# Kernel tuning notes

Hardware: AMD Instinct MI355X
Metric: run time of the kernel (lower is better)

Reference implementation:

```python
import jax, jax.numpy as jnp
import numpy as np

N_HEADS = 16
NEG_INF = -1e9


def setup_inputs() -> dict:
    key = jax.random.key(0)
    ks = jax.random.split(key, 8)
    B, S, D = 2, 2048, 1024
    HD = D // N_HEADS
    x = jax.random.normal(ks[0], (B, S, D), dtype=jnp.float32)
    # RoPE frequencies (llama-style): theta = 10000^(-2i/head_dim)
    inv_freq = 1.0 / (10000.0 ** (np.arange(0, HD, 2, dtype=np.float32) / HD))  # [HD//2]
    angles = np.arange(S, dtype=np.float32)[:, None] * inv_freq[None, :]        # [S, HD//2]
    freqs_cos = jnp.asarray(np.cos(angles))
    freqs_sin = jnp.asarray(np.sin(angles))
    # additive causal mask [1,1,S,S]
    mask = jnp.where(np.tril(np.ones((S, S), dtype=bool)), 0.0, NEG_INF).astype(jnp.float32)[None, None]
    scale = 0.02
    wq = jax.random.normal(ks[1], (D, D), dtype=jnp.float32) * scale
    wk = jax.random.normal(ks[2], (D, D), dtype=jnp.float32) * scale
    wv = jax.random.normal(ks[3], (D, D), dtype=jnp.float32) * scale
    wo = jax.random.normal(ks[4], (D, D), dtype=jnp.float32) * scale
    return {"x": x, "freqs_cos": freqs_cos, "freqs_sin": freqs_sin, "mask": mask,
            "wq": wq, "wk": wk, "wv": wv, "wo": wo}


def _rope(t, cos, sin):
    # t: [B,S,H,HD]; cos/sin: [S,HD//2]; complex mult (t0 + i t1) * (cos + i sin)
    b, s, h, hd = t.shape
    tr = t.reshape(b, s, h, hd // 2, 2)
    t0, t1 = tr[..., 0], tr[..., 1]
    c = cos[None, :, None, :]
    sn = sin[None, :, None, :]
    out = jnp.stack([t0 * c - t1 * sn, t0 * sn + t1 * c], axis=-1)
    return out.reshape(b, s, h, hd)


def reference(x, freqs_cos, freqs_sin, mask, wq, wk, wv, wo):
    b, s, d = x.shape
    hd = d // N_HEADS
    # torch Linear: y = x @ W.T
    xq = (x @ wq.T).reshape(b, s, N_HEADS, hd)
    xk = (x @ wk.T).reshape(b, s, N_HEADS, hd)
    xv = (x @ wv.T).reshape(b, s, N_HEADS, hd)
    xq = _rope(xq, freqs_cos, freqs_sin)
    xk = _rope(xk, freqs_cos, freqs_sin)
    # [B,H,S,S] scores
    scores = jnp.einsum('bqhd,bkhd->bhqk', xq, xk) / jnp.sqrt(jnp.asarray(hd, x.dtype))
    scores = scores + mask
    probs = jax.nn.softmax(scores.astype(jnp.float32), axis=-1).astype(x.dtype)
    out = jnp.einsum('bhqk,bkhd->bqhd', probs, xv).reshape(b, s, d)
    return out @ wo.T
```

## Files before the change

kernel.cpp:

```cpp
#include <hip/hip_runtime.h>
#include <hip/hip_bf16.h>
#include <cstdint>

typedef __attribute__((ext_vector_type(4))) float f32x4;
typedef __attribute__((ext_vector_type(8))) short s16x8;
typedef __attribute__((ext_vector_type(4))) unsigned short u16x4;
typedef unsigned short u16;
typedef unsigned int u32;
typedef unsigned long long u64;

__device__ __forceinline__ float b2f(u16 u){ u32 v = ((u32)u)<<16; return __builtin_bit_cast(float, v); }
__device__ __forceinline__ u16 f2b(float f){
  __hip_bfloat16 h = __float2bfloat16(f);
  return __builtin_bit_cast(u16, h);
}

__device__ __forceinline__ void gld16(const void* g, void* l){
  __builtin_amdgcn_global_load_lds((const __attribute__((address_space(1))) void*)g,
                                   (__attribute__((address_space(3))) void*)l, 16, 0, 0);
}

__device__ __forceinline__ f32x4 mfma16(s16x8 a, s16x8 b, f32x4 c){
  return __builtin_amdgcn_mfma_f32_16x16x32_bf16(a, b, c, 0, 0, 0);
}

#define WS_XB   0u
#define WS_WQ   (4u<<20)
#define WS_WK   (5u<<20)
#define WS_WV   (6u<<20)
#define WS_WO   (7u<<20)
#define WS_Q    (8u<<20)
#define WS_K    (12u<<20)
#define WS_VT   (16u<<20)
#define WS_AO   (20u<<20)

#define QSCALE 0.18033688f

__global__ __launch_bounds__(256) void k_convert(const float* __restrict__ x,
    const float* __restrict__ wq, const float* __restrict__ wk,
    const float* __restrict__ wv, const float* __restrict__ wo,
    u16* __restrict__ ws){
  u32 idx = blockIdx.x*256u + threadIdx.x;
  const float* src; u16* dst;
  if (idx < (1u<<20)) { src = x + (u64)idx*4u; dst = ws + WS_XB + (u64)idx*4u; }
  else {
    u32 widx = idx - (1u<<20);
    u32 wsel = widx >> 18;
    u32 off  = (widx & ((1u<<18)-1u)) * 4u;
    const float* sp = (wsel==0u)?wq:(wsel==1u)?wk:(wsel==2u)?wv:wo;
    src = sp + off; dst = ws + WS_WQ + (u64)wsel*(1u<<20) + off;
  }
  f32x4 v = *(const f32x4*)src;
  u16x4 o = { f2b(v[0]), f2b(v[1]), f2b(v[2]), f2b(v[3]) };
  *(u16x4*)dst = o;
}

__global__ __launch_bounds__(256,2) void k_gemm(u16* __restrict__ ws, float* __restrict__ out,
    const float* __restrict__ fc, const float* __restrict__ fs, int pass){
  __shared__ char sm[65536];
  const u32 tid = threadIdx.x;
  const u32 w = tid>>6, l = tid&63u, g = l>>4, li = l&15u;
  const u32 wr = w>>1, wc = w&1u;
  u32 bx = blockIdx.x;

  const u16 *Ap, *Bp; u32 arow0, brow0; int mode;
  if (pass == 0) {
    u32 seg = bx >> 8, b2 = bx & 255u;
    if (seg < 2u) {
      Ap = ws + WS_XB; Bp = ws + (seg ? WS_WK : WS_WQ);
      arow0 = (b2 >> 3) * 128u; brow0 = (b2 & 7u) * 128u; mode = (int)seg;
    } else {
      Ap = ws + WS_WV; Bp = ws + WS_XB;
      arow0 = (b2 >> 5) * 128u; brow0 = (b2 & 31u) * 128u; mode = 2;
    }
  } else {
    Ap = ws + WS_AO; Bp = ws + WS_WO;
    arow0 = (bx >> 3) * 128u; brow0 = (bx & 7u) * 128u; mode = 3;
  }

  f32x4 acc[4][4];
  #pragma unroll
  for (u32 m=0;m<4;++m)
    #pragma unroll
    for (u32 n=0;n<4;++n) acc[m][n] = 0.0f;

  auto STAGE_G = [&](u32 s, u32 t){
    const u32 k0 = t*64u;
    #pragma unroll
    for (u32 j = 0; j < 4u; ++j) {
      u32 p = w*4096u + j*1024u + l*16u;
      u32 row = p >> 7, colb = p & 127u;
      u32 cS = colb ^ ((row & 7u) << 4);
      gld16(Ap + (u64)(arow0 + row)*1024u + k0 + (cS>>1), sm + s*32768u + w*4096u + j*1024u);
      gld16(Bp + (u64)(brow0 + row)*1024u + k0 + (cS>>1), sm + s*32768u + 16384u + w*4096u + j*1024u);
    }
  };

  STAGE_G(0u, 0u);
  __syncthreads();

  u32 cur = 0u;
  for (u32 t = 0; t < 16u; ++t) {
    if (t + 1u < 16u) STAGE_G(cur^1u, t+1u);
    const u32 cb = cur*32768u;
    s16x8 af[2][4], bf[2][4];
    #pragma unroll
    for (u32 kk=0;kk<2u;++kk){
      #pragma unroll
      for (u32 m=0;m<4;++m){
        u32 row = wr*64u + m*16u + li;
        af[kk][m] = *(const s16x8*)(sm + cb + row*128u + ((kk*64u + g*16u) ^ ((row&7u)<<4)));
      }
      #pragma unroll
      for (u32 n=0;n<4;++n){
        u32 row = wc*64u + n*16u + li;
        bf[kk][n] = *(const s16x8*)(sm + cb + 16384u + row*128u + ((kk*64u + g*16u) ^ ((row&7u)<<4)));
      }
    }
    #pragma unroll
    for (u32 kk=0;kk<2u;++kk)
      #pragma unroll
      for (u32 m=0;m<4;++m)
        #pragma unroll
        for (u32 n=0;n<4;++n)
          acc[m][n] = mfma16(af[kk][m], bf[kk][n], acc[m][n]);
    __syncthreads();
    cur ^= 1u;
  }

  u16* qdst = ws + WS_Q; u16* kdst = ws + WS_K; u16* vtd = ws + WS_VT;
  if (mode <= 1) {
    #pragma unroll
    for (u32 m=0;m<4;++m)
      #pragma unroll
      for (u32 n=0;n<4;++n)
        #pragma unroll
        for (u32 q=0;q<4;++q){
          u32 row = wr*64u + m*16u + 4u*g + q;
          u32 colb = (wc*64u + n*16u + li)*2u;
          *(u16*)(sm + row*256u + (colb ^ ((row&7u)<<4))) = f2b(acc[m][n][q]);
        }
    __syncthreads();
    u32 row = tid >> 1, half = tid & 1u;
    u32 r = arow0 + row;
    u32 b = r >> 11, s = r & 2047u;
    u32 h = (brow0 >> 6) + half;
    float qs = (mode==0) ? QSCALE : 1.0f;
    u16* d = ((mode==0) ? qdst : kdst) + (u64)(((b<<4)+h)*2048u + s)*64u;
    #pragma unroll
    for (u32 u0=0; u0<8u; ++u0){
      s16x8 cv = *(const s16x8*)(sm + row*256u + ((half*128u + u0*16u) ^ ((row&7u)<<4)));
      f32x4 cvv = *(const f32x4*)(fc + s*32u + u0*4u);
      f32x4 svv = *(const f32x4*)(fs + s*32u + u0*4u);
      s16x8 o;
      #pragma unroll
      for (u32 i=0;i<4;++i){
        float t0 = b2f((u16)cv[2*i]), t1 = b2f((u16)cv[2*i+1]);
        o[2*i]   = (short)f2b((t0*cvv[i] - t1*svv[i])*qs);
        o[2*i+1] = (short)f2b((t0*svv[i] + t1*cvv[i])*qs);
      }
      *(s16x8*)(d + u0*8u) = o;
    }
  } else {
    #pragma unroll
    for (u32 m=0;m<4;++m){
      u32 r0 = arow0 + wr*64u + m*16u + 4u*g;
      #pragma unroll
      for (u32 n=0;n<4;++n){
        u32 c = brow0 + wc*64u + n*16u + li;
        #pragma unroll
        for (u32 q=0;q<4;++q){
          float v = acc[m][n][q];
          u32 r = r0 + q;
          if (mode == 2) vtd[(u64)r*4096u + c] = f2b(v);
          else           out[(u64)r*1024u + c] = v;
        }
      }
    }
  }
}

__global__ __launch_bounds__(256) void k_attn(u16* __restrict__ ws){
  __shared__ char sm[40960];
  const u32 tid = threadIdx.x;
  const u32 w = tid>>6, l = tid&63u, g = l>>4, li = l&15u;
  u32 bx = blockIdx.x;
  u32 qt = 31u - (bx >> 5);
  u32 bh = bx & 31u;
  u32 b = bh >> 4, h = bh & 15u;
  const u16* Q  = ws + WS_Q + (u64)bh*2048u*64u;
  const u16* Kp = ws + WS_K + (u64)bh*2048u*64u;
  const u16* Vt = ws + WS_VT + (u64)(h*64u)*4096u + b*2048u;
  u16* AO = ws + WS_AO;
  const u32 qw = qt*64u + w*16u;

  s16x8 qa[2];
  #pragma unroll
  for (u32 kk=0;kk<2;++kk)
    qa[kk] = *(const s16x8*)(Q + (u64)(qw + li)*64u + kk*32u + g*8u);

  s16x8 ones;
  #pragma unroll
  for (u32 i=0;i<8;++i) ones[i] = (short)0x3F80;

  f32x4 o[4]; f32x4 lsum;
  #pragma unroll
  for (u32 n=0;n<4;++n) o[n] = 0.0f;
  lsum = 0.0f;

  char* pl = sm + 32768 + w*2048u;
  const u32 nt = qt + 1u;

  auto STAGE = [&](u32 s, u32 kvb){
    #pragma unroll
    for (u32 j=0;j<2u;++j){
      u32 p = (w*2u+j)*1024u + l*16u;
      u32 row = p >> 7, colb = p & 127u;
      u32 cS = colb ^ ((row & 7u) << 4);
      gld16(Kp + (u64)(kvb + row)*64u + (cS>>1), sm + s*16384u + (w*2u+j)*1024u);
      gld16(Vt + (u64)row*4096u + kvb + (cS>>1), sm + s*16384u + 8192u + (w*2u+j)*1024u);
    }
  };

  STAGE(0u, 0u);
  __syncthreads();

  u32 cur = 0u;
  for (u32 t = 0; t < nt; ++t) {
    const u32 kvb = t*64u;
    if (t + 1u < nt) STAGE(cur^1u, kvb + 64u);
    const u32 cb = cur*16384u;

    f32x4 sv[4];
    #pragma unroll
    for (u32 n=0;n<4;++n) sv[n] = 0.0f;
    #pragma unroll
    for (u32 n=0;n<4;++n){
      u32 kvr = n*16u + li;
      #pragma unroll
      for (u32 kk=0;kk<2u;++kk){
        s16x8 kf = *(const s16x8*)(sm + cb + kvr*128u + ((kk*64u + g*16u) ^ ((kvr&7u)<<4)));
        sv[n] = mfma16(qa[kk], kf, sv[n]);
      }
    }
    if (t == nt - 1u) {
      #pragma unroll
      for (u32 n=0;n<4;++n)
        #pragma unroll
        for (u32 q=0;q<4;++q){
          u32 qr = qw + 4u*g + q;
          u32 kc = kvb + n*16u + li;
          if (kc > qr) sv[n][q] = -1e9f;
        }
    }
    #pragma unroll
    for (u32 n=0;n<4;++n)
      #pragma unroll
      for (u32 q=0;q<4;++q){
        u32 row = 4u*g + q;
        *(u16*)(pl + row*128u + (((n*16u + li)*2u) ^ ((row&7u)<<4))) = f2b(exp2f(sv[n][q]));
      }
    #pragma unroll
    for (u32 kk=0;kk<2u;++kk){
      s16x8 pa = *(const s16x8*)(pl + li*128u + ((kk*64u + g*16u) ^ ((li&7u)<<4)));
      lsum = mfma16(pa, ones, lsum);
      #pragma unroll
      for (u32 n=0;n<4;++n){
        u32 hr = n*16u + li;
        s16x8 vf = *(const s16x8*)(sm + cb + 8192u + hr*128u + ((kk*64u + g*16u) ^ ((hr&7u)<<4)));
        o[n] = mfma16(pa, vf, o[n]);
      }
    }
    __syncthreads();
    cur ^= 1u;
  }

  #pragma unroll
  for (u32 q=0;q<4;++q){
    float inv = 1.0f / lsum[q];
    u32 qr = qw + 4u*g + q;
    #pragma unroll
    for (u32 n=0;n<4;++n){
      u32 hd = n*16u + li;
      AO[((u64)(b*2048u + qr))*1024u + h*64u + hd] = f2b(o[n][q] * inv);
    }
  }
}

extern "C" void kernel_launch(void* const* d_in, const int* in_sizes, int n_in,
                              void* d_out, int out_size, void* d_ws, size_t ws_size,
                              hipStream_t stream) {
  const float* x  = (const float*)d_in[0];
  const float* fc = (const float*)d_in[1];
  const float* fs = (const float*)d_in[2];
  const float* wq = (const float*)d_in[4];
  const float* wk = (const float*)d_in[5];
  const float* wv = (const float*)d_in[6];
  const float* wo = (const float*)d_in[7];
  u16* ws = (u16*)d_ws;
  float* out = (float*)d_out;

  k_convert<<<8192, 256, 0, stream>>>(x, wq, wk, wv, wo, ws);
  k_gemm  <<<768,  256, 0, stream>>>(ws, out, fc, fs, 0);
  k_attn  <<<1024, 256, 0, stream>>>(ws);
  k_gemm  <<<256,  256, 0, stream>>>(ws, out, fc, fs, 1);
}
```

Baseline: 109.5 us.

## Split long causal attention rows across two blocks and merge partials

Query tiles 16-31 now have their KV range split into two halves, each processed by a separate block. This raises the attention grid from 1024 to 1536 blocks and evens out per-block work under the causal mask. Unnormalized partial outputs (bf16) and row sums go to workspace, and a new combine kernel sums them and normalizes. In exchange it adds a kernel launch, extra global traffic for the partials, and bf16 rounding of the partial outputs. It also reuses workspace regions (the start of ws and the WQ area) as scratch, assuming they are dead by this point.

```diff
diff --git a/kernel.cpp b/kernel.cpp
--- a/kernel.cpp
+++ b/kernel.cpp
@@ -185,8 +185,12 @@
   const u32 tid = threadIdx.x;
   const u32 w = tid>>6, l = tid&63u, g = l>>4, li = l&15u;
   u32 bx = blockIdx.x;
-  u32 qt = 31u - (bx >> 5);
+  u32 j = bx >> 5;
   u32 bh = bx & 31u;
+  u32 qt, t0, t1; bool split;
+  if (j < 16u)      { qt = 16u + j;  t0 = 0u;  t1 = 16u;      split = true;  }
+  else if (j < 32u) { qt = 47u - j;  t0 = 16u; t1 = qt + 1u;  split = true;  }
+  else              { qt = 47u - j;  t0 = 0u;  t1 = qt + 1u;  split = false; }
   u32 b = bh >> 4, h = bh & 15u;
   const u16* Q  = ws + WS_Q + (u64)bh*2048u*64u;
   const u16* Kp = ws + WS_K + (u64)bh*2048u*64u;
@@ -209,26 +213,25 @@
   lsum = 0.0f;
 
   char* pl = sm + 32768 + w*2048u;
-  const u32 nt = qt + 1u;
 
   auto STAGE = [&](u32 s, u32 kvb){
     #pragma unroll
-    for (u32 j=0;j<2u;++j){
-      u32 p = (w*2u+j)*1024u + l*16u;
+    for (u32 jj=0;jj<2u;++jj){
+      u32 p = (w*2u+jj)*1024u + l*16u;
       u32 row = p >> 7, colb = p & 127u;
       u32 cS = colb ^ ((row & 7u) << 4);
-      gld16(Kp + (u64)(kvb + row)*64u + (cS>>1), sm + s*16384u + (w*2u+j)*1024u);
-      gld16(Vt + (u64)row*4096u + kvb + (cS>>1), sm + s*16384u + 8192u + (w*2u+j)*1024u);
+      gld16(Kp + (u64)(kvb + row)*64u + (cS>>1), sm + s*16384u + (w*2u+jj)*1024u);
+      gld16(Vt + (u64)row*4096u + kvb + (cS>>1), sm + s*16384u + 8192u + (w*2u+jj)*1024u);
     }
   };
 
-  STAGE(0u, 0u);
+  STAGE(0u, t0*64u);
   __syncthreads();
 
   u32 cur = 0u;
-  for (u32 t = 0; t < nt; ++t) {
+  for (u32 t = t0; t < t1; ++t) {
     const u32 kvb = t*64u;
-    if (t + 1u < nt) STAGE(cur^1u, kvb + 64u);
+    if (t + 1u < t1) STAGE(cur^1u, kvb + 64u);
     const u32 cb = cur*16384u;
 
     f32x4 sv[4];
@@ -243,7 +246,7 @@
         sv[n] = mfma16(qa[kk], kf, sv[n]);
       }
     }
-    if (t == nt - 1u) {
+    if (t == qt) {
       #pragma unroll
       for (u32 n=0;n<4;++n)
         #pragma unroll
@@ -275,16 +278,51 @@
     cur ^= 1u;
   }
 
-  #pragma unroll
-  for (u32 q=0;q<4;++q){
-    float inv = 1.0f / lsum[q];
-    u32 qr = qw + 4u*g + q;
-    #pragma unroll
-    for (u32 n=0;n<4;++n){
-      u32 hd = n*16u + li;
-      AO[((u64)(b*2048u + qr))*1024u + h*64u + hd] = f2b(o[n][q] * inv);
-    }
-  }
+  if (split) {
+    u32 set = (bh*16u + (qt - 16u))*2u + (t0 ? 1u : 0u);
+    u16* po = ws + (u64)set*4096u;
+    float* plm = (float*)(ws + WS_WQ) + set*64u;
+    #pragma unroll
+    for (u32 q=0;q<4;++q){
+      u32 rl = w*16u + 4u*g + q;
+      #pragma unroll
+      for (u32 n=0;n<4;++n)
+        po[rl*64u + n*16u + li] = f2b(o[n][q]);
+      if (li == 0u) plm[rl] = lsum[q];
+    }
+  } else {
+    #pragma unroll
+    for (u32 q=0;q<4;++q){
+      float inv = 1.0f / lsum[q];
+      u32 qr = qw + 4u*g + q;
+      #pragma unroll
+      for (u32 n=0;n<4;++n){
+        u32 hd = n*16u + li;
+        AO[((u64)(b*2048u + qr))*1024u + h*64u + hd] = f2b(o[n][q] * inv);
+      }
+    }
+  }
+}
+
+__global__ __launch_bounds__(256) void k_combine(u16* __restrict__ ws){
+  u32 idx = blockIdx.x*256u + threadIdx.x;
+  u32 g8 = idx & 7u;
+  u32 r  = (idx >> 3) & 63u;
+  u32 s2 = idx >> 9;
+  const u16* poA = ws + (u64)(s2*2u)*4096u + r*64u + g8*8u;
+  const u16* poB = poA + 4096u;
+  const float* plm = (float*)(ws + WS_WQ);
+  float inv = 1.0f / (plm[(s2*2u)*64u + r] + plm[(s2*2u+1u)*64u + r]);
+  s16x8 a = *(const s16x8*)poA;
+  s16x8 c = *(const s16x8*)poB;
+  s16x8 o;
+  #pragma unroll
+  for (u32 i=0;i<8;++i)
+    o[i] = (short)f2b((b2f((u16)a[i]) + b2f((u16)c[i])) * inv);
+  u32 bh = s2 >> 4, qt = 16u + (s2 & 15u);
+  u32 b = bh >> 4, h = bh & 15u;
+  u32 qrow = qt*64u + r;
+  *(s16x8*)(ws + WS_AO + (u64)(b*2048u + qrow)*1024u + h*64u + g8*8u) = o;
 }
 
 extern "C" void kernel_launch(void* const* d_in, const int* in_sizes, int n_in,
@@ -301,7 +339,8 @@
   float* out = (float*)d_out;
 
   k_convert<<<8192, 256, 0, stream>>>(x, wq, wk, wv, wo, ws);
-  k_gemm  <<<768,  256, 0, stream>>>(ws, out, fc, fs, 0);
-  k_attn  <<<1024, 256, 0, stream>>>(ws);
-  k_gemm  <<<256,  256, 0, stream>>>(ws, out, fc, fs, 1);
-}
+  k_gemm   <<<768,  256, 0, stream>>>(ws, out, fc, fs, 0);
+  k_attn   <<<1536, 256, 0, stream>>>(ws);
+  k_combine<<<1024, 256, 0, stream>>>(ws);
+  k_gemm   <<<256,  256, 0, stream>>>(ws, out, fc, fs, 1);
+}
```

New measurement: 114.8 us. +4.8%, slower.

## Store K/V tiles in MFMA fragment order and transpose QK^T to pack P writes

Applied to the files above, without the earlier changes.

The K and V tiles are now staged into shared memory already laid out in MFMA fragment order, so each lane reads its fragment at a fixed lane*16 offset with no XOR swizzle arithmetic. The score MFMA swaps operands to compute S^T, letting each lane convert four probabilities with packed bf16 conversion and write them as one 8-byte store instead of sixteen 2-byte stores. Launch bounds add a minimum of 4 blocks per CU to limit register use. The risks are LDS bank conflicts in the new unswizzled layout, and register spills from holding all eight K fragments at once under the tighter occupancy bound.

```diff
diff --git a/kernel.cpp b/kernel.cpp
--- a/kernel.cpp
+++ b/kernel.cpp
@@ -5,6 +5,7 @@
 typedef __attribute__((ext_vector_type(4))) float f32x4;
 typedef __attribute__((ext_vector_type(8))) short s16x8;
 typedef __attribute__((ext_vector_type(4))) unsigned short u16x4;
+typedef __attribute__((ext_vector_type(2))) unsigned int u32x2;
 typedef unsigned short u16;
 typedef unsigned int u32;
 typedef unsigned long long u64;
@@ -180,7 +181,7 @@
   }
 }
 
-__global__ __launch_bounds__(256) void k_attn(u16* __restrict__ ws){
+__global__ __launch_bounds__(256,4) void k_attn(u16* __restrict__ ws){
   __shared__ char sm[40960];
   const u32 tid = threadIdx.x;
   const u32 w = tid>>6, l = tid&63u, g = l>>4, li = l&15u;
@@ -211,14 +212,20 @@
   char* pl = sm + 32768 + w*2048u;
   const u32 nt = qt + 1u;
 
+  const u32 f0 = w*2u;
+  u32 kof[2], vof[2];
+  #pragma unroll
+  for (u32 j=0;j<2u;++j){
+    u32 f = f0 + j;
+    kof[j] = ((f>>1)*16u + li)*64u  + (f&1u)*32u + g*8u;
+    vof[j] = ((f>>1)*16u + li)*4096u + (f&1u)*32u + g*8u;
+  }
   auto STAGE = [&](u32 s, u32 kvb){
     #pragma unroll
     for (u32 j=0;j<2u;++j){
-      u32 p = (w*2u+j)*1024u + l*16u;
-      u32 row = p >> 7, colb = p & 127u;
-      u32 cS = colb ^ ((row & 7u) << 4);
-      gld16(Kp + (u64)(kvb + row)*64u + (cS>>1), sm + s*16384u + (w*2u+j)*1024u);
-      gld16(Vt + (u64)row*4096u + kvb + (cS>>1), sm + s*16384u + 8192u + (w*2u+j)*1024u);
+      u32 f = f0 + j;
+      gld16(Kp + (u64)kvb*64u + kof[j], sm + s*16384u + f*1024u);
+      gld16(Vt + (u64)vof[j] + kvb,     sm + s*16384u + 8192u + f*1024u);
     }
   };
 
@@ -229,45 +236,47 @@
   for (u32 t = 0; t < nt; ++t) {
     const u32 kvb = t*64u;
     if (t + 1u < nt) STAGE(cur^1u, kvb + 64u);
-    const u32 cb = cur*16384u;
+    const char* kb = sm + cur*16384u + l*16u;
+
+    s16x8 kf[8];
+    #pragma unroll
+    for (u32 f=0; f<8u; ++f)
+      kf[f] = *(const s16x8*)(kb + f*1024u);
 
     f32x4 sv[4];
     #pragma unroll
     for (u32 n=0;n<4;++n) sv[n] = 0.0f;
     #pragma unroll
-    for (u32 n=0;n<4;++n){
-      u32 kvr = n*16u + li;
-      #pragma unroll
-      for (u32 kk=0;kk<2u;++kk){
-        s16x8 kf = *(const s16x8*)(sm + cb + kvr*128u + ((kk*64u + g*16u) ^ ((kvr&7u)<<4)));
-        sv[n] = mfma16(qa[kk], kf, sv[n]);
-      }
-    }
+    for (u32 n=0;n<4;++n)
+      #pragma unroll
+      for (u32 kk=0;kk<2u;++kk)
+        sv[n] = mfma16(kf[n*2u+kk], qa[kk], sv[n]);
+
     if (t == nt - 1u) {
       #pragma unroll
       for (u32 n=0;n<4;++n)
         #pragma unroll
-        for (u32 q=0;q<4;++q){
-          u32 qr = qw + 4u*g + q;
-          u32 kc = kvb + n*16u + li;
-          if (kc > qr) sv[n][q] = -1e9f;
-        }
-    }
-    #pragma unroll
-    for (u32 n=0;n<4;++n)
-      #pragma unroll
-      for (u32 q=0;q<4;++q){
-        u32 row = 4u*g + q;
-        *(u16*)(pl + row*128u + (((n*16u + li)*2u) ^ ((row&7u)<<4))) = f2b(exp2f(sv[n][q]));
-      }
+        for (u32 r=0;r<4;++r)
+          if (kvb + n*16u + 4u*g + r > qw + li) sv[n][r] = -1e9f;
+    }
+    #pragma unroll
+    for (u32 n=0;n<4;++n){
+      f32x4 p;
+      #pragma unroll
+      for (u32 r=0;r<4;++r) p[r] = exp2f(sv[n][r]);
+      u32 w0, w1;
+      asm("v_cvt_pk_bf16_f32 %0, %1, %2" : "=v"(w0) : "v"(p[0]), "v"(p[1]));
+      asm("v_cvt_pk_bf16_f32 %0, %1, %2" : "=v"(w1) : "v"(p[2]), "v"(p[3]));
+      u32x2 pw = { w0, w1 };
+      *(u32x2*)(pl + li*128u + ((n*32u + g*8u) ^ ((li&7u)<<4))) = pw;
+    }
     #pragma unroll
     for (u32 kk=0;kk<2u;++kk){
       s16x8 pa = *(const s16x8*)(pl + li*128u + ((kk*64u + g*16u) ^ ((li&7u)<<4)));
       lsum = mfma16(pa, ones, lsum);
       #pragma unroll
       for (u32 n=0;n<4;++n){
-        u32 hr = n*16u + li;
-        s16x8 vf = *(const s16x8*)(sm + cb + 8192u + hr*128u + ((kk*64u + g*16u) ^ ((hr&7u)<<4)));
+        s16x8 vf = *(const s16x8*)(kb + 8192u + (n*2u+kk)*1024u);
         o[n] = mfma16(pa, vf, o[n]);
       }
     }
@@ -276,13 +285,13 @@
   }
 
   #pragma unroll
-  for (u32 q=0;q<4;++q){
-    float inv = 1.0f / lsum[q];
-    u32 qr = qw + 4u*g + q;
+  for (u32 r=0;r<4;++r){
+    float inv = 1.0f / lsum[r];
+    u32 qr = qw + 4u*g + r;
     #pragma unroll
     for (u32 n=0;n<4;++n){
       u32 hd = n*16u + li;
-      AO[((u64)(b*2048u + qr))*1024u + h*64u + hd] = f2b(o[n][q] * inv);
+      AO[((u64)(b*2048u + qr))*1024u + h*64u + hd] = f2b(o[n][r] * inv);
     }
   }
 }
```

Result: no change. 111.1 us (+1.5%).
